# Optimization experiments

Hardware: AMD Instinct MI355X
Metric: run time of the kernel (lower is better)

## Reference

```python
import jax, jax.numpy as jnp
import numpy as np

S, B, I, H = 2048, 64, 256, 512


def setup_inputs() -> dict:
    key = jax.random.key(0)
    ks = jax.random.split(key, 13)
    f = lambda k, sh: jax.random.normal(k, sh, dtype=jnp.float32) * 0.05
    m = lambda k, sh: jax.random.randint(k, sh, 0, 2, dtype=jnp.int32)
    return {
        "x": f(ks[0], (S, B, I)),
        "W_ih0": f(ks[1], (H, I)),
        "W_hh0": f(ks[2], (H, H)),
        "b_ih0": f(ks[3], (H,)),
        "b_hh0": f(ks[4], (H,)),
        "W_ih1": f(ks[5], (H, H)),
        "W_hh1": f(ks[6], (H, H)),
        "b_ih1": f(ks[7], (H,)),
        "b_hh1": f(ks[8], (H,)),
        "mask_ih0": m(ks[9], (H, I)),
        "mask_hh0": m(ks[10], (H, H)),
        "mask_ih1": m(ks[11], (H, H)),
        "mask_hh1": m(ks[12], (H, H)),
    }


def _rnn_layer(x, Wih, Whh, bih, bhh):
    # x: [S, B, in]; tanh RNN layer, h0 = zeros. Precompute input projection
    # for all timesteps (one big GEMM), then scan the recurrence.
    xb = jnp.einsum('sbi,hi->sbh', x, Wih) + bih + bhh  # [S, B, H]

    def step(h, xt):
        h = jnp.tanh(xt + h @ Whh.T)
        return h, h

    h0 = jnp.zeros((x.shape[1], Whh.shape[0]), dtype=x.dtype)
    _, ys = jax.lax.scan(step, h0, xb)
    return ys  # [S, B, H]


def reference(x, W_ih0, W_hh0, b_ih0, b_hh0, W_ih1, W_hh1, b_ih1, b_hh1,
              mask_ih0, mask_hh0, mask_ih1, mask_hh1):
    dt = x.dtype
    y0 = _rnn_layer(x,
                    W_ih0 * mask_ih0.astype(dt), W_hh0 * mask_hh0.astype(dt),
                    b_ih0, b_hh0)
    y1 = _rnn_layer(y0,
                    W_ih1 * mask_ih1.astype(dt), W_hh1 * mask_hh1.astype(dt),
                    b_ih1, b_hh1)
    return y1[-1]  # last timestep hidden state: [B, H]
```

## Files before the change

### kernel.cpp

```cpp
#include <hip/hip_runtime.h>
#include <math.h>

typedef unsigned int u32;
typedef unsigned long long u64;
typedef unsigned short u16;
typedef __attribute__((ext_vector_type(8))) short short8;
typedef __attribute__((ext_vector_type(4))) float f4;
typedef __attribute__((ext_vector_type(4))) u32 u32x4;

#define Ssz 2048
#define Bsz 64
#define Isz 256
#define Hsz 512
#define NBLK 256
#define KC0 24
#define KC1 32

#define WB0_OFF   0u
#define WB1_OFF   1572864u
#define BIAS0_OFF 3670016u
#define BIAS1_OFF 3672064u
#define CNT_OFF   3674112u
#define H0_OFF    3674368u
#define H1_OFF    3936512u

#define MFMA(a, b, c) __builtin_amdgcn_mfma_f32_16x16x32_bf16(a, b, c, 0, 0, 0)

__device__ __forceinline__ u16 f2bf(float f) {
  union { float f; u32 u; } v; v.f = f;
  u32 r = v.u + 0x7FFFu + ((v.u >> 16) & 1u);
  return (u16)(r >> 16);
}
__device__ __forceinline__ float bf2f(u16 h) {
  union { u32 u; float f; } v; v.u = ((u32)h) << 16;
  return v.f;
}
__device__ __forceinline__ u32 packbf(float f) {
  u16 hi = f2bf(f);
  u16 lo = f2bf(f - bf2f(hi));
  return (u32)hi | ((u32)lo << 16);
}
__device__ __forceinline__ void unpack2(u32 w0, u32 w1, u32& hi, u32& lo) {
  hi = __builtin_amdgcn_perm(w1, w0, 0x05040100u);
  lo = __builtin_amdgcn_perm(w1, w0, 0x07060302u);
}
__device__ __forceinline__ void cvt2(float a, float b, u32& hi, u32& lo) {
  u16 ha = f2bf(a), hb = f2bf(b);
  u16 la = f2bf(a - bf2f(ha)), lb = f2bf(b - bf2f(hb));
  hi = (u32)ha | ((u32)hb << 16);
  lo = (u32)la | ((u32)lb << 16);
}

union frag { short8 s; u32 w[4]; };

__global__ void prep_weights(const float* __restrict__ Wih0, const float* __restrict__ Whh0,
                             const float* __restrict__ bih0, const float* __restrict__ bhh0,
                             const float* __restrict__ Wih1, const float* __restrict__ Whh1,
                             const float* __restrict__ bih1, const float* __restrict__ bhh1,
                             const int* __restrict__ mih0, const int* __restrict__ mhh0,
                             const int* __restrict__ mih1, const int* __restrict__ mhh1,
                             char* __restrict__ ws) {
  const int L0E = 768 * 512, L1E = 1024 * 512;
  int e = blockIdx.x * blockDim.x + threadIdx.x;
  if (e >= L0E + L1E + 1024) return;
  if (e < L0E) {
    int f = e >> 9, fe = e & 511;
    int lane = fe >> 3, j = fe & 7;
    int n = lane & 15, q = lane >> 4;
    int nt = f / KC0, kc = f % KC0;
    int u = nt * 16 + n, k = kc * 32 + q * 8 + j;
    float w;
    if (k < 256) w = Wih0[u * 256 + k] * (float)mih0[u * 256 + k];
    else         w = Whh0[u * 512 + (k - 256)] * (float)mhh0[u * 512 + (k - 256)];
    ((u32*)(ws + WB0_OFF))[e] = packbf(w);
  } else if (e < L0E + L1E) {
    int e1 = e - L0E;
    int f = e1 >> 9, fe = e1 & 511;
    int lane = fe >> 3, j = fe & 7;
    int n = lane & 15, q = lane >> 4;
    int nt = f >> 5, kc = f & 31;
    int u = nt * 16 + n, k = kc * 32 + q * 8 + j;
    float w;
    if (k < 512) w = Wih1[u * 512 + k] * (float)mih1[u * 512 + k];
    else         w = Whh1[u * 512 + (k - 512)] * (float)mhh1[u * 512 + (k - 512)];
    ((u32*)(ws + WB1_OFF))[e1] = packbf(w);
  } else {
    int b2 = e - L0E - L1E;
    if (b2 < 512) ((float*)(ws + BIAS0_OFF))[b2] = bih0[b2] + bhh0[b2];
    else          ((float*)(ws + BIAS1_OFF))[b2 - 512] = bih1[b2 - 512] + bhh1[b2 - 512];
  }
}

__device__ __forceinline__ void gbar(u32* cnt, int tid, u32 target, bool wait) {
  asm volatile("" ::: "memory");
  __syncthreads();
  if (tid == 0) {
    __hip_atomic_fetch_add(cnt, 1u, __ATOMIC_RELAXED, __HIP_MEMORY_SCOPE_AGENT);
    if (wait) {
      while (__hip_atomic_load(cnt, __ATOMIC_RELAXED, __HIP_MEMORY_SCOPE_AGENT) < target)
        __builtin_amdgcn_s_sleep(1);
    }
  }
  __syncthreads();
  asm volatile("" ::: "memory");
}

template <int L>
__device__ __forceinline__ void epilogue(f4 acc, float* red, float bs, int tid, int b0, int nt,
                                         u32* H0, u32* H1, float* out, int t) {
  const int lane = tid & 63, wid = tid >> 6;
  *(f4*)&red[(wid << 8) + lane * 4] = acc;
  __syncthreads();
  float sum = red[tid] + red[256 + tid] + red[512 + tid] + red[768 + tid];
  const int l = tid >> 2, r = tid & 3;
  const int m = ((l >> 4) << 2) + r;
  const int u = nt * 16 + (l & 15);
  const int b = b0 + m;
  float val = tanhf(bs + sum);
  u32 pv = packbf(val);
  if (L == 0) {
    __hip_atomic_store(H0 + (t & 1) * 32768 + b * Hsz + u, pv,
                       __ATOMIC_RELAXED, __HIP_MEMORY_SCOPE_AGENT);
  } else {
    __hip_atomic_store(H1 + ((t - 1) & 1) * 32768 + b * Hsz + u, pv,
                       __ATOMIC_RELAXED, __HIP_MEMORY_SCOPE_AGENT);
    if (t == Ssz) out[b * Hsz + u] = val;
  }
}

__device__ __forceinline__ void run0(const float* __restrict__ x, char* __restrict__ ws,
                                     float* __restrict__ out, int b0, int nt, int tid, float* red) {
  const int lane = tid & 63, wid = tid >> 6;
  const int n = lane & 15, q = lane >> 4;
  const u32* WB = (const u32*)(ws + WB0_OFF);
  u32* cnt = (u32*)(ws + CNT_OFF);
  u32* H0 = (u32*)(ws + H0_OFF);
  u32* H1 = (u32*)(ws + H1_OFF);
  const float bs = ((const float*)(ws + BIAS0_OFF))[nt * 16 + ((tid >> 2) & 15)];

  short8 Whi[6], Wlo[6];
  #pragma unroll
  for (int i = 0; i < 6; ++i) {
    int kcg = wid + 4 * i;
    const u32* p = WB + ((nt * KC0 + kcg) * 64 + lane) * 8;
    u32x4 a = *(const u32x4*)p;
    u32x4 b = *(const u32x4*)(p + 4);
    frag h, l;
    unpack2(a.x, a.y, h.w[0], l.w[0]);
    unpack2(a.z, a.w, h.w[1], l.w[1]);
    unpack2(b.x, b.y, h.w[2], l.w[2]);
    unpack2(b.z, b.w, h.w[3], l.w[3]);
    Whi[i] = h.s; Wlo[i] = l.s;
  }

  f4 xp[2][2];
  auto loadx = [&](int t) {
    const float* xb = x + ((long)t * Bsz + b0 + n) * Isz + q * 8;
    #pragma unroll
    for (int i = 0; i < 2; ++i) {
      int kcg = wid + 4 * i;
      xp[i][0] = *(const f4*)(xb + kcg * 32);
      xp[i][1] = *(const f4*)(xb + kcg * 32 + 4);
    }
  };
  loadx(0);

  for (int t = 0; t < Ssz; ++t) {
    short8 Axh[2], Axl[2];
    #pragma unroll
    for (int i = 0; i < 2; ++i) {
      frag h, l;
      #pragma unroll
      for (int v = 0; v < 2; ++v) {
        f4 f = xp[i][v];
        cvt2(f.x, f.y, h.w[2 * v], l.w[2 * v]);
        cvt2(f.z, f.w, h.w[2 * v + 1], l.w[2 * v + 1]);
      }
      Axh[i] = h.s; Axl[i] = l.s;
    }
    const u32* Hp = H0 + ((t - 1) & 1) * 32768 + (b0 + n) * Hsz + q * 8;
    u64 hb[4][4];
    #pragma unroll
    for (int i = 0; i < 4; ++i) {
      const u64* p = (const u64*)(Hp + (wid + 4 * i) * 32);
      #pragma unroll
      for (int v = 0; v < 4; ++v)
        hb[i][v] = __hip_atomic_load(p + v, __ATOMIC_RELAXED, __HIP_MEMORY_SCOPE_AGENT);
    }
    f4 acc = {0.f, 0.f, 0.f, 0.f};
    #pragma unroll
    for (int i = 0; i < 2; ++i) {
      acc = MFMA(Axh[i], Whi[i], acc);
      acc = MFMA(Axh[i], Wlo[i], acc);
      acc = MFMA(Axl[i], Whi[i], acc);
    }
    #pragma unroll
    for (int i = 0; i < 4; ++i) {
      frag h, l;
      #pragma unroll
      for (int v = 0; v < 4; ++v) {
        u32 w0 = (u32)hb[i][v], w1 = (u32)(hb[i][v] >> 32);
        unpack2(w0, w1, h.w[v], l.w[v]);
      }
      acc = MFMA(h.s, Whi[i + 2], acc);
      acc = MFMA(h.s, Wlo[i + 2], acc);
      acc = MFMA(l.s, Whi[i + 2], acc);
    }
    loadx(t + 1 < Ssz ? t + 1 : 0);
    epilogue<0>(acc, red, bs, tid, b0, nt, H0, H1, out, t);
    gbar(cnt, tid, (u32)NBLK * (u32)(t + 1), t + 1 < Ssz);
  }
}

__device__ __forceinline__ void run1(char* __restrict__ ws, float* __restrict__ out,
                                     int b0, int nt, int tid, float* red) {
  const int lane = tid & 63, wid = tid >> 6;
  const int n = lane & 15, q = lane >> 4;
  const u32* WB = (const u32*)(ws + WB1_OFF);
  u32* cnt = (u32*)(ws + CNT_OFF);
  u32* H0 = (u32*)(ws + H0_OFF);
  u32* H1 = (u32*)(ws + H1_OFF);
  const float bs = ((const float*)(ws + BIAS1_OFF))[nt * 16 + ((tid >> 2) & 15)];

  short8 Whi[8], Wlo[8];
  #pragma unroll
  for (int i = 0; i < 8; ++i) {
    int kcg = wid + 4 * i;
    const u32* p = WB + ((nt * KC1 + kcg) * 64 + lane) * 8;
    u32x4 a = *(const u32x4*)p;
    u32x4 b = *(const u32x4*)(p + 4);
    frag h, l;
    unpack2(a.x, a.y, h.w[0], l.w[0]);
    unpack2(a.z, a.w, h.w[1], l.w[1]);
    unpack2(b.x, b.y, h.w[2], l.w[2]);
    unpack2(b.z, b.w, h.w[3], l.w[3]);
    Whi[i] = h.s; Wlo[i] = l.s;
  }

  gbar(cnt, tid, (u32)NBLK, true);
  for (int t = 1; t <= Ssz; ++t) {
    const u32* base0 = H0 + ((t - 1) & 1) * 32768 + (b0 + n) * Hsz + q * 8;
    const u32* base1 = H1 + (t & 1) * 32768 + (b0 + n) * Hsz + q * 8;
    u64 hb[8][4];
    #pragma unroll
    for (int i = 0; i < 8; ++i) {
      const u32* bp = (i < 4) ? base0 : base1;
      const u64* p = (const u64*)(bp + (wid + 4 * (i & 3)) * 32);
      #pragma unroll
      for (int v = 0; v < 4; ++v)
        hb[i][v] = __hip_atomic_load(p + v, __ATOMIC_RELAXED, __HIP_MEMORY_SCOPE_AGENT);
    }
    f4 acc = {0.f, 0.f, 0.f, 0.f};
    #pragma unroll
    for (int i = 0; i < 8; ++i) {
      frag h, l;
      #pragma unroll
      for (int v = 0; v < 4; ++v) {
        u32 w0 = (u32)hb[i][v], w1 = (u32)(hb[i][v] >> 32);
        unpack2(w0, w1, h.w[v], l.w[v]);
      }
      acc = MFMA(h.s, Whi[i], acc);
      acc = MFMA(h.s, Wlo[i], acc);
      acc = MFMA(l.s, Whi[i], acc);
    }
    epilogue<1>(acc, red, bs, tid, b0, nt, H0, H1, out, t);
    gbar(cnt, tid, (u32)NBLK * (u32)(t + 1), t < Ssz);
  }
}

__global__ __launch_bounds__(256, 1) void rnn_persist(const float* __restrict__ x,
                                                      char* __restrict__ ws,
                                                      float* __restrict__ out) {
  __shared__ float red[1024];
  const int tid = threadIdx.x;
  const int wg = blockIdx.x;
  const int b0 = ((wg >> 5) & 3) * 16;
  const int nt = wg & 31;
  if (wg < 128) run0(x, ws, out, b0, nt, tid, red);
  else          run1(ws, out, b0, nt, tid, red);
}

extern "C" void kernel_launch(void* const* d_in, const int* in_sizes, int n_in,
                              void* d_out, int out_size, void* d_ws, size_t ws_size,
                              hipStream_t stream) {
  const float* x    = (const float*)d_in[0];
  const float* Wih0 = (const float*)d_in[1];
  const float* Whh0 = (const float*)d_in[2];
  const float* bih0 = (const float*)d_in[3];
  const float* bhh0 = (const float*)d_in[4];
  const float* Wih1 = (const float*)d_in[5];
  const float* Whh1 = (const float*)d_in[6];
  const float* bih1 = (const float*)d_in[7];
  const float* bhh1 = (const float*)d_in[8];
  const int* mih0   = (const int*)d_in[9];
  const int* mhh0   = (const int*)d_in[10];
  const int* mih1   = (const int*)d_in[11];
  const int* mhh1   = (const int*)d_in[12];
  char* ws = (char*)d_ws;

  hipMemsetAsync(ws + CNT_OFF, 0, 524544, stream);

  const int tot = 768 * 512 + 1024 * 512 + 1024;
  prep_weights<<<(tot + 255) / 256, 256, 0, stream>>>(
      Wih0, Whh0, bih0, bhh0, Wih1, Whh1, bih1, bhh1,
      mih0, mhh0, mih1, mhh1, ws);

  rnn_persist<<<NBLK, 256, 0, stream>>>(x, ws, (float*)d_out);
}
```

Measured before the change: 16.62 ms.

## Replace global barrier with per-batch-group flag sync and wider blocks

Replaces the grid-wide atomic counter barrier with per-batch-group flag arrays, so each block waits only on the producers it depends on (layer 0 step t-1 and layer 1 step t-2), letting the two layers pipeline independently across batch groups. Blocks grow to 512 threads with 8 waves splitting K into halves, the grid shrinks to 64 blocks, hidden-state buffers move to a triple-buffered tiled layout, and the x projection MFMAs are issued before polling. It also swaps tanhf for an exp-based fast tanh. This adds polling traffic on several flags and more registers per thread, and the fast tanh may lose some accuracy.

```diff
diff --git a/kernel.cpp b/kernel.cpp
--- a/kernel.cpp
+++ b/kernel.cpp
@@ -12,7 +12,6 @@
 #define Bsz 64
 #define Isz 256
 #define Hsz 512
-#define NBLK 256
 #define KC0 24
 #define KC1 32
 
@@ -20,9 +19,9 @@
 #define WB1_OFF   1572864u
 #define BIAS0_OFF 3670016u
 #define BIAS1_OFF 3672064u
-#define CNT_OFF   3674112u
-#define H0_OFF    3674368u
-#define H1_OFF    3936512u
+#define FLAGS_OFF 3674112u
+#define H0_OFF    3675136u
+#define H1_OFF    4068352u
 
 #define MFMA(a, b, c) __builtin_amdgcn_mfma_f32_16x16x32_bf16(a, b, c, 0, 0, 0)
 
@@ -50,8 +49,44 @@
   hi = (u32)ha | ((u32)hb << 16);
   lo = (u32)la | ((u32)lb << 16);
 }
+__device__ __forceinline__ float ftanh(float xx) {
+  float x = fminf(20.f, fmaxf(-20.f, xx));
+  float e = __expf(2.f * x);
+  return (e - 1.f) / (e + 1.f);
+}
 
 union frag { short8 s; u32 w[4]; };
+
+__device__ __forceinline__ u64 ald64(const u64* p) {
+  return __hip_atomic_load(p, __ATOMIC_RELAXED, __HIP_MEMORY_SCOPE_AGENT);
+}
+__device__ __forceinline__ u32 ald32(const u32* p) {
+  return __hip_atomic_load(p, __ATOMIC_RELAXED, __HIP_MEMORY_SCOPE_AGENT);
+}
+__device__ __forceinline__ void ast32(u32* p, u32 v) {
+  __hip_atomic_store(p, v, __ATOMIC_RELAXED, __HIP_MEMORY_SCOPE_AGENT);
+}
+
+__device__ __forceinline__ void poll1(const u32* f, int tgt) {
+  if (tgt <= 0) return;
+  while (1) {
+    int ok = 1;
+    #pragma unroll
+    for (int i = 0; i < 8; ++i) ok &= ((int)ald32(f + i) >= tgt);
+    if (ok) break;
+  }
+}
+__device__ __forceinline__ void poll2(const u32* f0, int t0, const u32* f1, int t1) {
+  if (t0 <= 0 && t1 <= 0) return;
+  while (1) {
+    int ok = 1;
+    #pragma unroll
+    for (int i = 0; i < 8; ++i) ok &= ((int)ald32(f0 + i) >= t0);
+    #pragma unroll
+    for (int i = 0; i < 8; ++i) ok &= ((int)ald32(f1 + i) >= t1);
+    if (ok) break;
+  }
+}
 
 __global__ void prep_weights(const float* __restrict__ Wih0, const float* __restrict__ Whh0,
                              const float* __restrict__ bih0, const float* __restrict__ bhh0,
@@ -91,60 +126,24 @@
   }
 }
 
-__device__ __forceinline__ void gbar(u32* cnt, int tid, u32 target, bool wait) {
-  asm volatile("" ::: "memory");
-  __syncthreads();
-  if (tid == 0) {
-    __hip_atomic_fetch_add(cnt, 1u, __ATOMIC_RELAXED, __HIP_MEMORY_SCOPE_AGENT);
-    if (wait) {
-      while (__hip_atomic_load(cnt, __ATOMIC_RELAXED, __HIP_MEMORY_SCOPE_AGENT) < target)
-        __builtin_amdgcn_s_sleep(1);
-    }
-  }
-  __syncthreads();
-  asm volatile("" ::: "memory");
-}
-
-template <int L>
-__device__ __forceinline__ void epilogue(f4 acc, float* red, float bs, int tid, int b0, int nt,
-                                         u32* H0, u32* H1, float* out, int t) {
-  const int lane = tid & 63, wid = tid >> 6;
-  *(f4*)&red[(wid << 8) + lane * 4] = acc;
-  __syncthreads();
-  float sum = red[tid] + red[256 + tid] + red[512 + tid] + red[768 + tid];
-  const int l = tid >> 2, r = tid & 3;
-  const int m = ((l >> 4) << 2) + r;
-  const int u = nt * 16 + (l & 15);
-  const int b = b0 + m;
-  float val = tanhf(bs + sum);
-  u32 pv = packbf(val);
-  if (L == 0) {
-    __hip_atomic_store(H0 + (t & 1) * 32768 + b * Hsz + u, pv,
-                       __ATOMIC_RELAXED, __HIP_MEMORY_SCOPE_AGENT);
-  } else {
-    __hip_atomic_store(H1 + ((t - 1) & 1) * 32768 + b * Hsz + u, pv,
-                       __ATOMIC_RELAXED, __HIP_MEMORY_SCOPE_AGENT);
-    if (t == Ssz) out[b * Hsz + u] = val;
-  }
-}
 
 __device__ __forceinline__ void run0(const float* __restrict__ x, char* __restrict__ ws,
-                                     float* __restrict__ out, int b0, int nt, int tid, float* red) {
-  const int lane = tid & 63, wid = tid >> 6;
-  const int n = lane & 15, q = lane >> 4;
+                                     int m, int p, int tid, float (*red)[256]) {
+  const int w = tid >> 6, lane = tid & 63, n = lane & 15, q = lane >> 4;
+  const int nt = p * 4 + (w & 3), ks = w >> 2;
+  const int b0 = m * 16;
   const u32* WB = (const u32*)(ws + WB0_OFF);
-  u32* cnt = (u32*)(ws + CNT_OFF);
-  u32* H0 = (u32*)(ws + H0_OFF);
-  u32* H1 = (u32*)(ws + H1_OFF);
-  const float bs = ((const float*)(ws + BIAS0_OFF))[nt * 16 + ((tid >> 2) & 15)];
-
-  short8 Whi[6], Wlo[6];
+  u32* flags0 = (u32*)(ws + FLAGS_OFF + m * 256);
+  u32* flags1 = flags0 + 16;
+  const float bs = ((const float*)(ws + BIAS0_OFF))[nt * 16 + n];
+
+  short8 Whi[12], Wlo[12];
   #pragma unroll
-  for (int i = 0; i < 6; ++i) {
-    int kcg = wid + 4 * i;
-    const u32* p = WB + ((nt * KC0 + kcg) * 64 + lane) * 8;
-    u32x4 a = *(const u32x4*)p;
-    u32x4 b = *(const u32x4*)(p + 4);
+  for (int i = 0; i < 12; ++i) {
+    const int kcg = 2 * i + ks;
+    const u32* pw = WB + ((nt * KC0 + kcg) * 64 + lane) * 8;
+    u32x4 a = *(const u32x4*)pw;
+    u32x4 b = *(const u32x4*)(pw + 4);
     frag h, l;
     unpack2(a.x, a.y, h.w[0], l.w[0]);
     unpack2(a.z, a.w, h.w[1], l.w[1]);
@@ -153,22 +152,20 @@
     Whi[i] = h.s; Wlo[i] = l.s;
   }
 
-  f4 xp[2][2];
+  f4 xp[4][2];
   auto loadx = [&](int t) {
-    const float* xb = x + ((long)t * Bsz + b0 + n) * Isz + q * 8;
-    #pragma unroll
-    for (int i = 0; i < 2; ++i) {
-      int kcg = wid + 4 * i;
-      xp[i][0] = *(const f4*)(xb + kcg * 32);
-      xp[i][1] = *(const f4*)(xb + kcg * 32 + 4);
+    #pragma unroll
+    for (int i = 0; i < 4; ++i) {
+      const int kcg = 2 * i + ks;
+      const float* sx = x + ((long)t * Bsz + b0 + n) * Isz + kcg * 32 + q * 8;
+      xp[i][0] = *(const f4*)sx;
+      xp[i][1] = *(const f4*)(sx + 4);
     }
   };
-  loadx(0);
-
-  for (int t = 0; t < Ssz; ++t) {
-    short8 Axh[2], Axl[2];
-    #pragma unroll
-    for (int i = 0; i < 2; ++i) {
+  short8 Axh[4], Axl[4];
+  auto cvtx = [&]() {
+    #pragma unroll
+    for (int i = 0; i < 4; ++i) {
       frag h, l;
       #pragma unroll
       for (int v = 0; v < 2; ++v) {
@@ -178,57 +175,77 @@
       }
       Axh[i] = h.s; Axl[i] = l.s;
     }
-    const u32* Hp = H0 + ((t - 1) & 1) * 32768 + (b0 + n) * Hsz + q * 8;
-    u64 hb[4][4];
+  };
+  loadx(0); cvtx();
+
+  const int cst = (nt * 16 + n) >> 5;
+  const int qp = ((nt * 2) + (n >> 3)) & 3;
+  const int jj = n & 7;
+
+  for (int t = 0; t < Ssz; ++t) {
+    f4 acc = {0.f, 0.f, 0.f, 0.f};
     #pragma unroll
     for (int i = 0; i < 4; ++i) {
-      const u64* p = (const u64*)(Hp + (wid + 4 * i) * 32);
-      #pragma unroll
-      for (int v = 0; v < 4; ++v)
-        hb[i][v] = __hip_atomic_load(p + v, __ATOMIC_RELAXED, __HIP_MEMORY_SCOPE_AGENT);
-    }
-    f4 acc = {0.f, 0.f, 0.f, 0.f};
-    #pragma unroll
-    for (int i = 0; i < 2; ++i) {
       acc = MFMA(Axh[i], Whi[i], acc);
       acc = MFMA(Axh[i], Wlo[i], acc);
       acc = MFMA(Axl[i], Whi[i], acc);
     }
-    #pragma unroll
-    for (int i = 0; i < 4; ++i) {
+    if (tid == 0) poll2(flags0, t, flags1, t - 2);
+    __syncthreads();
+    const u32* rb = (const u32*)(ws + H0_OFF) + (((t + 2) % 3) * 4 + m) * 8192;
+    u64 hb[8][4];
+    #pragma unroll
+    for (int i = 0; i < 8; ++i) {
+      const u64* pp = (const u64*)(rb + (2 * i + ks) * 512 + lane * 8);
+      #pragma unroll
+      for (int v = 0; v < 4; ++v) hb[i][v] = ald64(pp + v);
+    }
+    loadx(t + 1 < Ssz ? t + 1 : t);
+    #pragma unroll
+    for (int i = 0; i < 8; ++i) {
       frag h, l;
       #pragma unroll
-      for (int v = 0; v < 4; ++v) {
-        u32 w0 = (u32)hb[i][v], w1 = (u32)(hb[i][v] >> 32);
-        unpack2(w0, w1, h.w[v], l.w[v]);
-      }
-      acc = MFMA(h.s, Whi[i + 2], acc);
-      acc = MFMA(h.s, Wlo[i + 2], acc);
-      acc = MFMA(l.s, Whi[i + 2], acc);
-    }
-    loadx(t + 1 < Ssz ? t + 1 : 0);
-    epilogue<0>(acc, red, bs, tid, b0, nt, H0, H1, out, t);
-    gbar(cnt, tid, (u32)NBLK * (u32)(t + 1), t + 1 < Ssz);
+      for (int v = 0; v < 4; ++v)
+        unpack2((u32)hb[i][v], (u32)(hb[i][v] >> 32), h.w[v], l.w[v]);
+      acc = MFMA(h.s, Whi[4 + i], acc);
+      acc = MFMA(h.s, Wlo[4 + i], acc);
+      acc = MFMA(l.s, Whi[4 + i], acc);
+    }
+    *(f4*)&red[w][lane * 4] = acc;
+    __syncthreads();
+    if (w < 4) {
+      u32* wb = (u32*)(ws + H0_OFF) + ((t % 3) * 4 + m) * 8192;
+      f4 s0 = *(f4*)&red[w][lane * 4];
+      f4 s1 = *(f4*)&red[w + 4][lane * 4];
+      #pragma unroll
+      for (int r = 0; r < 4; ++r) {
+        float val = ftanh(bs + s0[r] + s1[r]);
+        ast32(wb + cst * 512 + ((q * 4 + r) + 16 * qp) * 8 + jj, packbf(val));
+      }
+    }
+    __syncthreads();
+    if (tid == 0) ast32(flags0 + p, (u32)(t + 1));
+    cvtx();
   }
 }
 
 __device__ __forceinline__ void run1(char* __restrict__ ws, float* __restrict__ out,
-                                     int b0, int nt, int tid, float* red) {
-  const int lane = tid & 63, wid = tid >> 6;
-  const int n = lane & 15, q = lane >> 4;
+                                     int m, int p, int tid, float (*red)[256]) {
+  const int w = tid >> 6, lane = tid & 63, n = lane & 15, q = lane >> 4;
+  const int nt = p * 4 + (w & 3), ks = w >> 2;
+  const int b0 = m * 16;
   const u32* WB = (const u32*)(ws + WB1_OFF);
-  u32* cnt = (u32*)(ws + CNT_OFF);
-  u32* H0 = (u32*)(ws + H0_OFF);
-  u32* H1 = (u32*)(ws + H1_OFF);
-  const float bs = ((const float*)(ws + BIAS1_OFF))[nt * 16 + ((tid >> 2) & 15)];
-
-  short8 Whi[8], Wlo[8];
+  u32* flags0 = (u32*)(ws + FLAGS_OFF + m * 256);
+  u32* flags1 = flags0 + 16;
+  const float bs = ((const float*)(ws + BIAS1_OFF))[nt * 16 + n];
+
+  short8 Whi[16], Wlo[16];
   #pragma unroll
-  for (int i = 0; i < 8; ++i) {
-    int kcg = wid + 4 * i;
-    const u32* p = WB + ((nt * KC1 + kcg) * 64 + lane) * 8;
-    u32x4 a = *(const u32x4*)p;
-    u32x4 b = *(const u32x4*)(p + 4);
+  for (int i = 0; i < 16; ++i) {
+    const int kcg = 2 * i + ks;
+    const u32* pw = WB + ((nt * KC1 + kcg) * 64 + lane) * 8;
+    u32x4 a = *(const u32x4*)pw;
+    u32x4 b = *(const u32x4*)(pw + 4);
     frag h, l;
     unpack2(a.x, a.y, h.w[0], l.w[0]);
     unpack2(a.z, a.w, h.w[1], l.w[1]);
@@ -237,47 +254,83 @@
     Whi[i] = h.s; Wlo[i] = l.s;
   }
 
-  gbar(cnt, tid, (u32)NBLK, true);
+  const int cst = (nt * 16 + n) >> 5;
+  const int qp = ((nt * 2) + (n >> 3)) & 3;
+  const int jj = n & 7;
+
   for (int t = 1; t <= Ssz; ++t) {
-    const u32* base0 = H0 + ((t - 1) & 1) * 32768 + (b0 + n) * Hsz + q * 8;
-    const u32* base1 = H1 + (t & 1) * 32768 + (b0 + n) * Hsz + q * 8;
-    u64 hb[8][4];
-    #pragma unroll
-    for (int i = 0; i < 8; ++i) {
-      const u32* bp = (i < 4) ? base0 : base1;
-      const u64* p = (const u64*)(bp + (wid + 4 * (i & 3)) * 32);
-      #pragma unroll
-      for (int v = 0; v < 4; ++v)
-        hb[i][v] = __hip_atomic_load(p + v, __ATOMIC_RELAXED, __HIP_MEMORY_SCOPE_AGENT);
-    }
+    if (tid == 0) poll1(flags1, t - 1);
+    __syncthreads();
     f4 acc = {0.f, 0.f, 0.f, 0.f};
-    #pragma unroll
-    for (int i = 0; i < 8; ++i) {
-      frag h, l;
-      #pragma unroll
-      for (int v = 0; v < 4; ++v) {
-        u32 w0 = (u32)hb[i][v], w1 = (u32)(hb[i][v] >> 32);
-        unpack2(w0, w1, h.w[v], l.w[v]);
-      }
-      acc = MFMA(h.s, Whi[i], acc);
-      acc = MFMA(h.s, Wlo[i], acc);
-      acc = MFMA(l.s, Whi[i], acc);
-    }
-    epilogue<1>(acc, red, bs, tid, b0, nt, H0, H1, out, t);
-    gbar(cnt, tid, (u32)NBLK * (u32)(t + 1), t < Ssz);
-  }
-}
-
-__global__ __launch_bounds__(256, 1) void rnn_persist(const float* __restrict__ x,
+    {
+      const u32* rb = (const u32*)(ws + H1_OFF) + ((t & 1) * 4 + m) * 8192;
+      u64 hb[8][4];
+      #pragma unroll
+      for (int i = 0; i < 8; ++i) {
+        const u64* pp = (const u64*)(rb + (2 * i + ks) * 512 + lane * 8);
+        #pragma unroll
+        for (int v = 0; v < 4; ++v) hb[i][v] = ald64(pp + v);
+      }
+      #pragma unroll
+      for (int i = 0; i < 8; ++i) {
+        frag h, l;
+        #pragma unroll
+        for (int v = 0; v < 4; ++v)
+          unpack2((u32)hb[i][v], (u32)(hb[i][v] >> 32), h.w[v], l.w[v]);
+        acc = MFMA(h.s, Whi[8 + i], acc);
+        acc = MFMA(h.s, Wlo[8 + i], acc);
+        acc = MFMA(l.s, Whi[8 + i], acc);
+      }
+    }
+    if (tid == 0) poll1(flags0, t);
+    __syncthreads();
+    {
+      const u32* rb = (const u32*)(ws + H0_OFF) + (((t - 1) % 3) * 4 + m) * 8192;
+      u64 hb[8][4];
+      #pragma unroll
+      for (int i = 0; i < 8; ++i) {
+        const u64* pp = (const u64*)(rb + (2 * i + ks) * 512 + lane * 8);
+        #pragma unroll
+        for (int v = 0; v < 4; ++v) hb[i][v] = ald64(pp + v);
+      }
+      #pragma unroll
+      for (int i = 0; i < 8; ++i) {
+        frag h, l;
+        #pragma unroll
+        for (int v = 0; v < 4; ++v)
+          unpack2((u32)hb[i][v], (u32)(hb[i][v] >> 32), h.w[v], l.w[v]);
+        acc = MFMA(h.s, Whi[i], acc);
+        acc = MFMA(h.s, Wlo[i], acc);
+        acc = MFMA(l.s, Whi[i], acc);
+      }
+    }
+    *(f4*)&red[w][lane * 4] = acc;
+    __syncthreads();
+    if (w < 4) {
+      u32* wb = (u32*)(ws + H1_OFF) + (((t - 1) & 1) * 4 + m) * 8192;
+      f4 s0 = *(f4*)&red[w][lane * 4];
+      f4 s1 = *(f4*)&red[w + 4][lane * 4];
+      #pragma unroll
+      for (int r = 0; r < 4; ++r) {
+        float val = ftanh(bs + s0[r] + s1[r]);
+        ast32(wb + cst * 512 + ((q * 4 + r) + 16 * qp) * 8 + jj, packbf(val));
+        if (t == Ssz) out[(b0 + q * 4 + r) * Hsz + nt * 16 + n] = val;
+      }
+    }
+    __syncthreads();
+    if (tid == 0) ast32(flags1 + p, (u32)t);
+  }
+}
+
+__global__ __launch_bounds__(512, 2) void rnn_persist(const float* __restrict__ x,
                                                       char* __restrict__ ws,
                                                       float* __restrict__ out) {
-  __shared__ float red[1024];
+  __shared__ float red[8][256];
   const int tid = threadIdx.x;
   const int wg = blockIdx.x;
-  const int b0 = ((wg >> 5) & 3) * 16;
-  const int nt = wg & 31;
-  if (wg < 128) run0(x, ws, out, b0, nt, tid, red);
-  else          run1(ws, out, b0, nt, tid, red);
+  const int m = (wg >> 3) & 3, p = wg & 7;
+  if (wg < 32) run0(x, ws, m, p, tid, red);
+  else         run1(ws, out, m, p, tid, red);
 }
 
 extern "C" void kernel_launch(void* const* d_in, const int* in_sizes, int n_in,
@@ -298,12 +351,12 @@
   const int* mhh1   = (const int*)d_in[12];
   char* ws = (char*)d_ws;
 
-  hipMemsetAsync(ws + CNT_OFF, 0, 524544, stream);
+  hipMemsetAsync(ws + FLAGS_OFF, 0, 1024 + 393216 + 262144, stream);
 
   const int tot = 768 * 512 + 1024 * 512 + 1024;
   prep_weights<<<(tot + 255) / 256, 256, 0, stream>>>(
       Wih0, Whh0, bih0, bhh0, Wih1, Whh1, bih1, bhh1,
       mih0, mhh0, mih1, mhh1, ws);
 
-  rnn_persist<<<NBLK, 256, 0, stream>>>(x, ws, (float*)d_out);
-}
+  rnn_persist<<<64, 512, 0, stream>>>(x, ws, (float*)d_out);
+}
```

Result: no change. 16.54 ms (-0.5%).
